# Optimization experiments

Hardware: AMD Instinct MI355X
Metric: run time of the kernel (lower is better)

The kernel has to match this reference:

```python
import jax, jax.numpy as jnp
import numpy as np

IMAGE_SIZE = 224
FMAP_H = FMAP_W = 26   # resnet18 layer2 (28x28) after AvgPool2d(3, stride=1)
N_REWEIGHT = 3
SIGMA = 4.0
KSIZE = 2 * int(4.0 * SIGMA + 0.5) + 1  # 33, kornia-style default kernel for sigma=4


def _gaussian_kernel1d():
    x = np.arange(KSIZE, dtype=np.float64) - (KSIZE - 1) / 2.0
    k = np.exp(-0.5 * (x / SIGMA) ** 2)
    return jnp.asarray((k / k.sum()).astype(np.float32))


def _cdist(x, y):
    # Euclidean cdist: x [N,D], y [M,D] -> [N,M], via the expanded quadratic form.
    x2 = jnp.sum(x * x, axis=1, keepdims=True)          # [N,1]
    y2 = jnp.sum(y * y, axis=1)                          # [M]
    d2 = x2 + y2 - 2.0 * (x @ y.T)                       # [N,M]
    return jnp.sqrt(jnp.maximum(d2, 0.0))


def _gaussian_blur(img):
    # Separable depthwise gaussian blur with reflect padding, img [1,1,H,W].
    k1d = _gaussian_kernel1d()
    pad = (KSIZE - 1) // 2
    x = jnp.pad(img, ((0, 0), (0, 0), (pad, pad), (pad, pad)), mode='reflect')
    kh = k1d.reshape(1, 1, KSIZE, 1)
    kw = k1d.reshape(1, 1, 1, KSIZE)
    dn = ('NCHW', 'OIHW', 'NCHW')
    x = jax.lax.conv_general_dilated(x, kh, (1, 1), 'VALID', dimension_numbers=dn)
    x = jax.lax.conv_general_dilated(x, kw, (1, 1), 'VALID', dimension_numbers=dn)
    return x


def setup_inputs() -> dict:
    key = jax.random.key(0)
    k1, k2 = jax.random.split(key)
    patch = jax.random.normal(k1, (FMAP_H * FMAP_W, 384), dtype=jnp.float32)      # [676, 384]
    patch_lib = jax.random.normal(k2, (100000, 384), dtype=jnp.float32)            # coreset bank
    return {"patch": patch, "patch_lib": patch_lib}


def reference(patch, patch_lib):
    # dist = torch.cdist(patch, patch_lib); min over memory bank
    dist = _cdist(patch, patch_lib)                      # [N, M]
    min_val = jnp.min(dist, axis=1)                      # [N]
    min_idx = jnp.argmin(dist, axis=1)                   # [N]
    s_idx = jnp.argmax(min_val)                          # most anomalous patch
    s_star = min_val[s_idx]
    m_test = patch[s_idx]                                # [D]
    m_star = patch_lib[min_idx[s_idx]]                   # [D]
    # reweighting: k nearest neighbors of m_star in the bank (smallest distances)
    w_dist = jnp.linalg.norm(m_star[None, :] - patch_lib, axis=1)   # [M]
    _, nn_idx = jax.lax.top_k(-w_dist, N_REWEIGHT)                  # indices of k smallest
    m_star_knn = jnp.linalg.norm(m_test[None, :] - patch_lib[nn_idx[1:]], axis=1)  # [k-1]
    D = jnp.sqrt(jnp.asarray(patch.shape[1], dtype=jnp.float32))
    w = 1.0 - jnp.exp(s_star / D) / jnp.sum(jnp.exp(m_star_knn / D))
    s = w * s_star
    # segmentation map: reshape, bilinear upsample (align_corners=False), gaussian blur
    s_map = min_val.reshape(1, 1, FMAP_H, FMAP_W)
    s_map = jax.image.resize(s_map, (1, 1, IMAGE_SIZE, IMAGE_SIZE), method='bilinear')
    s_map = _gaussian_blur(s_map)
    return s, s_map
```

## Files before the change

### kernel.cpp

```cpp
#include <hip/hip_runtime.h>

#define M_PATCH 676
#define K_DIM   384
#define N_LIB   100000
#define BM      128
#define BN      128
#define NCH     782
#define MTILES  6
#define M_PAD   (MTILES*BM)
#define N_PAD   (NCH*BN)
#define XCHUNK  98
#define GRID_GEMM (8*XCHUNK*MTILES)
#define NTOPB   1563
#define NCAND   (NTOPB*3)
#define IMG     224
#define FMAP    26
#define KS      33
#define KHALF   16

typedef __attribute__((ext_vector_type(4))) float  f32x4;
typedef __attribute__((ext_vector_type(8))) short  short8;
typedef unsigned long long ull;

static __device__ __forceinline__ unsigned short f2bf(float f) {
  unsigned u = __float_as_uint(f);
  u = u + 0x7FFFu + ((u >> 16) & 1u);
  return (unsigned short)(u >> 16);
}

static __device__ __forceinline__ ull shfl_xor_u64(ull v, int m) {
  unsigned lo = (unsigned)v, hi = (unsigned)(v >> 32);
  lo = __shfl_xor(lo, m, 64);
  hi = __shfl_xor(hi, m, 64);
  return ((ull)hi << 32) | lo;
}

static __device__ __forceinline__ ull umin64(ull a, ull b) { return a < b ? a : b; }
static __device__ __forceinline__ ull umax64(ull a, ull b) { return a > b ? a : b; }

static __device__ __forceinline__ void gld16(const unsigned short* g, unsigned short* l) {
  __builtin_amdgcn_global_load_lds(
      (const __attribute__((address_space(1))) void*)g,
      (__attribute__((address_space(3))) void*)l, 16, 0, 0);
}

__global__ void pc_norms_cvt_kernel(const float* __restrict__ patch, const float* __restrict__ lib,
                                    float* __restrict__ y2, float* __restrict__ x2,
                                    unsigned short* __restrict__ Abf, unsigned short* __restrict__ Bbf) {
  const int w = threadIdx.x >> 6, lane = threadIdx.x & 63;
  const long r = (long)blockIdx.x * 4 + w;
  if (r < N_PAD) {
    float s;
    if (r < N_LIB) {
      const float2* p = (const float2*)(lib + r * K_DIM);
      ushort2* q = (ushort2*)(Bbf + r * K_DIM);
      float2 v[3];
      s = 0.f;
      #pragma unroll
      for (int j = 0; j < 3; ++j) { v[j] = p[lane + 64 * j]; s += v[j].x * v[j].x + v[j].y * v[j].y; }
      #pragma unroll
      for (int j = 0; j < 3; ++j) q[lane + 64 * j] = make_ushort2(f2bf(v[j].x), f2bf(v[j].y));
      #pragma unroll
      for (int m = 1; m < 64; m <<= 1) s += __shfl_xor(s, m, 64);
    } else {
      s = __builtin_inff();
      ushort2* q = (ushort2*)(Bbf + r * K_DIM);
      #pragma unroll
      for (int j = 0; j < 3; ++j) q[lane + 64 * j] = make_ushort2(0, 0);
    }
    if (lane == 0) y2[r] = s;
  } else {
    const long pr = r - N_PAD;
    if (pr < M_PATCH) {
      const float2* p = (const float2*)(patch + pr * K_DIM);
      ushort2* q = (ushort2*)(Abf + pr * K_DIM);
      float2 v[3]; float s = 0.f;
      #pragma unroll
      for (int j = 0; j < 3; ++j) { v[j] = p[lane + 64 * j]; s += v[j].x * v[j].x + v[j].y * v[j].y; }
      #pragma unroll
      for (int j = 0; j < 3; ++j) q[lane + 64 * j] = make_ushort2(f2bf(v[j].x), f2bf(v[j].y));
      #pragma unroll
      for (int m = 1; m < 64; m <<= 1) s += __shfl_xor(s, m, 64);
      if (lane == 0) x2[pr] = s;
    } else if (pr < M_PAD) {
      ushort2* q = (ushort2*)(Abf + pr * K_DIM);
      #pragma unroll
      for (int j = 0; j < 3; ++j) q[lane + 64 * j] = make_ushort2(0, 0);
    }
  }
}

__launch_bounds__(256, 4)
__global__ void pc_gemm_min_bf16_kernel(const unsigned short* __restrict__ Abf,
                                        const unsigned short* __restrict__ Bbf,
                                        const float* __restrict__ x2g, const float* __restrict__ y2g,
                                        ull* __restrict__ partial) {
  __shared__ unsigned short As[2][BM * 32];
  __shared__ unsigned short Bs[2][BN * 32];
  __shared__ float x2s[BM];
  __shared__ float y2s[BN];
  __shared__ ull red[BM * 2];

  const int l = blockIdx.x;
  const int xcd = l & 7, slot = l >> 3;
  const int chunk = xcd * XCHUNK + slot / MTILES;
  const int mtile = slot % MTILES;
  if (chunk >= NCH) return;

  const int t = threadIdx.x;
  const int m0 = mtile * BM;
  const int n0 = chunk * BN;
  const int wid = t >> 6, lane = t & 63;

  if (t < BM) {
    const int gm = m0 + t;
    x2s[t] = (gm < M_PATCH) ? x2g[gm] : 0.f;
    y2s[t] = y2g[n0 + t];
  }

  const int srow   = (wid << 4) + (lane >> 2);
  const int spiece = (lane & 3) ^ ((lane >> 4) & 3);
  const unsigned short* gA0 = Abf + (size_t)(m0 + srow) * K_DIM + spiece * 8;
  const unsigned short* gA1 = gA0 + (size_t)64 * K_DIM;
  const unsigned short* gB0 = Bbf + (size_t)(n0 + srow) * K_DIM + spiece * 8;
  const unsigned short* gB1 = gB0 + (size_t)64 * K_DIM;

  f32x4 acc[4][4];
  #pragma unroll
  for (int i = 0; i < 4; ++i)
    #pragma unroll
    for (int j = 0; j < 4; ++j) acc[i][j] = (f32x4){0.f, 0.f, 0.f, 0.f};

  const int wm = wid >> 1, wn = wid & 1;
  const int quad = lane >> 4, l15 = lane & 15;
  const int poff = (quad ^ ((l15 >> 2) & 3)) * 8;

  for (int ks = 0; ks < K_DIM / 64; ++ks) {
    __syncthreads();
    #pragma unroll
    for (int h = 0; h < 2; ++h) {
      const int ko = ks * 64 + h * 32;
      gld16(gA0 + ko, &As[h][wid * 512]);
      gld16(gA1 + ko, &As[h][(wid + 4) * 512]);
      gld16(gB0 + ko, &Bs[h][wid * 512]);
      gld16(gB1 + ko, &Bs[h][(wid + 4) * 512]);
    }
    __builtin_amdgcn_s_waitcnt(0);
    __syncthreads();

    #pragma unroll
    for (int h = 0; h < 2; ++h) {
      short8 af[4], bf[4];
      #pragma unroll
      for (int mi = 0; mi < 4; ++mi)
        af[mi] = *(const short8*)&As[h][(wm * 64 + mi * 16 + l15) * 32 + poff];
      #pragma unroll
      for (int ni = 0; ni < 4; ++ni)
        bf[ni] = *(const short8*)&Bs[h][(wn * 64 + ni * 16 + l15) * 32 + poff];
      #pragma unroll
      for (int mi = 0; mi < 4; ++mi)
        #pragma unroll
        for (int ni = 0; ni < 4; ++ni)
          acc[mi][ni] = __builtin_amdgcn_mfma_f32_16x16x32_bf16(af[mi], bf[ni], acc[mi][ni], 0, 0, 0);
    }
  }

  #pragma unroll
  for (int mi = 0; mi < 4; ++mi) {
    #pragma unroll
    for (int r = 0; r < 4; ++r) {
      const int row_l = wm * 64 + mi * 16 + quad * 4 + r;
      const float xs = x2s[row_l];
      ull kmin = ~0ull;
      #pragma unroll
      for (int ni = 0; ni < 4; ++ni) {
        const int col_l = wn * 64 + ni * 16 + l15;
        float d2 = xs + y2s[col_l] - 2.0f * acc[mi][ni][r];
        d2 = fmaxf(d2, 0.0f);
        const ull key = ((ull)__float_as_uint(d2) << 32) | (unsigned)(n0 + col_l);
        kmin = umin64(kmin, key);
      }
      #pragma unroll
      for (int off = 1; off < 16; off <<= 1) kmin = umin64(kmin, shfl_xor_u64(kmin, off));
      if (l15 == 0) red[row_l * 2 + wn] = kmin;
    }
  }
  __syncthreads();
  if (t < BM) {
    const ull k = umin64(red[t * 2], red[t * 2 + 1]);
    partial[(size_t)chunk * M_PAD + m0 + t] = k;
  }
}

__global__ void pc_reduce_kernel(const ull* __restrict__ partial, ull* __restrict__ stage1,
                                 float* __restrict__ minval, unsigned* __restrict__ minidx,
                                 unsigned* __restrict__ scal) {
  const int b = blockIdx.x, mt = b >> 3, gp = b & 7;
  const int t = threadIdx.x;
  const int c0 = gp * XCHUNK;
  ull k = ~0ull;
  #pragma unroll 7
  for (int i = 0; i < XCHUNK; ++i)
    k = umin64(k, partial[(size_t)(c0 + i) * M_PAD + mt * 128 + t]);
  stage1[(size_t)(mt * 128 + t) * 8 + gp] = k;
  __threadfence();
  __syncthreads();
  __shared__ unsigned rank_s;
  if (t == 0) rank_s = atomicAdd(&scal[8], 1u);
  __syncthreads();
  if (rank_s != 47) return;
  __threadfence();

  ull best = 0ull;
  for (int m = t; m < M_PATCH; m += 128) {
    ull kk = ~0ull;
    #pragma unroll
    for (int g = 0; g < 8; ++g) kk = umin64(kk, stage1[(size_t)m * 8 + g]);
    const float d = sqrtf(fmaxf(__uint_as_float((unsigned)(kk >> 32)), 0.f));
    minval[m] = d;
    minidx[m] = (unsigned)kk;
    best = umax64(best, ((ull)__float_as_uint(d) << 32) | (0xFFFFFFFFu - (unsigned)m));
  }
  #pragma unroll
  for (int off = 1; off < 64; off <<= 1) best = umax64(best, shfl_xor_u64(best, off));
  __shared__ ull sh[2];
  if ((t & 63) == 0) sh[t >> 6] = best;
  __syncthreads();
  if (t == 0) {
    best = umax64(sh[0], sh[1]);
    const unsigned m = 0xFFFFFFFFu - (unsigned)best;
    scal[0] = m;
    scal[1] = (unsigned)(best >> 32);
    scal[2] = minidx[m];
  }
}

__global__ void pc_wdist_scan_kernel(const unsigned short* __restrict__ Bbf,
                                     const float* __restrict__ y2,
                                     const unsigned* __restrict__ scal,
                                     ull* __restrict__ cand) {
  __shared__ ull keys[64];
  const int t = threadIdx.x, w = t >> 6, lane = t & 63;
  const unsigned star = scal[2];
  const float y2star = y2[star];
  const unsigned* msp = (const unsigned*)(Bbf + (size_t)star * K_DIM);
  float msl[3], msh[3];
  #pragma unroll
  for (int j = 0; j < 3; ++j) {
    const unsigned u = msp[lane + 64 * j];
    msl[j] = __uint_as_float(u << 16);
    msh[j] = __uint_as_float(u & 0xFFFF0000u);
  }
  const long r0 = (long)blockIdx.x * 64 + w * 16;
  for (int i = 0; i < 16; ++i) {
    const long r = r0 + i;
    ull key = ~0ull;
    if (r < N_LIB) {
      const unsigned* p = (const unsigned*)(Bbf + (size_t)r * K_DIM);
      float s = 0.f;
      #pragma unroll
      for (int j = 0; j < 3; ++j) {
        const unsigned u = p[lane + 64 * j];
        s += msl[j] * __uint_as_float(u << 16) + msh[j] * __uint_as_float(u & 0xFFFF0000u);
      }
      #pragma unroll
      for (int m = 1; m < 64; m <<= 1) s += __shfl_xor(s, m, 64);
      const float d2 = fmaxf(y2star + y2[r] - 2.0f * s, 0.0f);
      key = ((ull)__float_as_uint(d2) << 32) | (unsigned)r;
    }
    if (lane == 0) keys[w * 16 + i] = key;
  }
  __syncthreads();
  if (t == 0) {
    ull picks[3];
    #pragma unroll
    for (int p = 0; p < 3; ++p) {
      ull best = ~0ull;
      for (int i = 0; i < 64; ++i) {
        const ull k = keys[i];
        if ((p > 0 && k == picks[0]) || (p > 1 && k == picks[1])) continue;
        best = umin64(best, k);
      }
      picks[p] = best;
      cand[(long)blockIdx.x * 3 + p] = best;
    }
  }
}

__global__ void pc_merge_final_kernel(const float* __restrict__ patch, const float* __restrict__ lib,
                                      const unsigned* __restrict__ scal, const ull* __restrict__ cand,
                                      float* __restrict__ out) {
  __shared__ ull shm[16];
  __shared__ ull picks_s[3];
  const int t = threadIdx.x, w = t >> 6, lane = t & 63;
  for (int p = 0; p < 3; ++p) {
    const ull e0 = (p > 0) ? picks_s[0] : 0ull;
    const ull e1 = (p > 1) ? picks_s[1] : 0ull;
    ull k = ~0ull;
    for (int n = t; n < NCAND; n += 1024) {
      const ull c = cand[n];
      if ((p > 0 && c == e0) || (p > 1 && c == e1)) continue;
      k = umin64(k, c);
    }
    #pragma unroll
    for (int off = 1; off < 64; off <<= 1) k = umin64(k, shfl_xor_u64(k, off));
    if ((t & 63) == 0) shm[t >> 6] = k;
    __syncthreads();
    if (t == 0) {
      #pragma unroll
      for (int ww = 1; ww < 16; ++ww) k = umin64(k, shm[ww]);
      picks_s[p] = k;
    }
    __syncthreads();
  }
  __shared__ float sh2[2];
  if (w < 2) {
    const unsigned nn = (unsigned)picks_s[1 + w];
    const float* mt2 = patch + (size_t)scal[0] * K_DIM;
    const float* pv  = lib + (size_t)nn * K_DIM;
    float s = 0.f;
    #pragma unroll
    for (int j = 0; j < 6; ++j) { const float d = mt2[lane + 64 * j] - pv[lane + 64 * j]; s += d * d; }
    #pragma unroll
    for (int m = 1; m < 64; m <<= 1) s += __shfl_xor(s, m, 64);
    if (lane == 0) sh2[w] = s;
  }
  __syncthreads();
  if (t == 0) {
    const float D = sqrtf((float)K_DIM);
    const float s_star = __uint_as_float(scal[1]);
    const float a = sqrtf(sh2[0]), b = sqrtf(sh2[1]);
    const float wgt = 1.f - expf(s_star / D) / (expf(a / D) + expf(b / D));
    out[0] = wgt * s_star;
  }
}

static __device__ __forceinline__ int pc_refl(int i) {
  return i < 0 ? -i : (i >= IMG ? 2 * IMG - 2 - i : i);
}

__global__ void pc_map_kernel(const float* __restrict__ minval, float* __restrict__ outmap) {
  __shared__ double kd[KS + 1];
  __shared__ float kf[KS];
  __shared__ float smap[FMAP * FMAP];
  __shared__ float by[IMG];
  const int t = threadIdx.x;
  const int y = blockIdx.x;
  if (t < KS) { const double xx = (double)(t - KHALF) / 4.0; kd[t] = exp(-0.5 * xx * xx); }
  for (int i = t; i < FMAP * FMAP; i += 256) smap[i] = minval[i];
  __syncthreads();
  if (t == 0) { double s = 0.0; for (int i = 0; i < KS; ++i) s += kd[i]; kd[KS] = s; }
  __syncthreads();
  if (t < KS) kf[t] = (float)(kd[t] / kd[KS]);
  __syncthreads();

  const float scale = (float)FMAP / (float)IMG;
  if (t < IMG) {
    const float fx = ((float)t + 0.5f) * scale - 0.5f;
    const int ix0 = (int)floorf(fx); const float tx = fx - (float)ix0;
    const int x0 = min(max(ix0, 0), FMAP - 1), x1 = min(max(ix0 + 1, 0), FMAP - 1);
    float s = 0.f;
    #pragma unroll
    for (int j = 0; j < KS; ++j) {
      const int yy = pc_refl(y + j - KHALF);
      const float fy = ((float)yy + 0.5f) * scale - 0.5f;
      const int iy0 = (int)floorf(fy); const float ty = fy - (float)iy0;
      const int y0 = min(max(iy0, 0), FMAP - 1), y1 = min(max(iy0 + 1, 0), FMAP - 1);
      const float v00 = smap[y0 * FMAP + x0], v01 = smap[y0 * FMAP + x1];
      const float v10 = smap[y1 * FMAP + x0], v11 = smap[y1 * FMAP + x1];
      const float v0 = v00 + (v01 - v00) * tx;
      const float v1 = v10 + (v11 - v10) * tx;
      s += kf[j] * (v0 + (v1 - v0) * ty);
    }
    by[t] = s;
  }
  __syncthreads();
  if (t < IMG) {
    float s = 0.f;
    #pragma unroll
    for (int i = 0; i < KS; ++i) s += kf[i] * by[pc_refl(t + i - KHALF)];
    outmap[y * IMG + t] = s;
  }
}

extern "C" void kernel_launch(void* const* d_in, const int* in_sizes, int n_in,
                              void* d_out, int out_size, void* d_ws, size_t ws_size,
                              hipStream_t stream) {
  const float* patch = (const float*)d_in[0];
  const float* lib   = (const float*)d_in[1];
  float* out = (float*)d_out;

  char* p = (char*)d_ws;
  auto take = [&](size_t n) { char* q = p; p += (n + 511) & ~(size_t)511; return q; };
  float* y2        = (float*)take((size_t)N_PAD * 4);
  float* x2        = (float*)take((size_t)M_PAD * 4);
  ull* partial     = (ull*)take((size_t)(NCH + 2) * M_PAD * 8);
  ull* stage1      = (ull*)take((size_t)M_PAD * 8 * 8);
  float* minval    = (float*)take((size_t)M_PATCH * 4);
  unsigned* minidx = (unsigned*)take((size_t)M_PATCH * 4);
  unsigned* scal   = (unsigned*)take(256);
  ull* cand        = (ull*)take((size_t)NCAND * 8);
  unsigned short* Abf = (unsigned short*)take((size_t)M_PAD * K_DIM * 2);
  unsigned short* Bbf = (unsigned short*)take((size_t)N_PAD * K_DIM * 2);
  (void)in_sizes; (void)n_in; (void)out_size; (void)ws_size;

  hipMemsetAsync(scal, 0, 64, stream);
  hipMemsetAsync(partial + (size_t)NCH * M_PAD, 0xFF, 2 * M_PAD * 8, stream);

  const int norm_rows = N_PAD + M_PAD;
  pc_norms_cvt_kernel<<<(norm_rows + 3) / 4, 256, 0, stream>>>(patch, lib, y2, x2, Abf, Bbf);
  pc_gemm_min_bf16_kernel<<<GRID_GEMM, 256, 0, stream>>>(Abf, Bbf, x2, y2, partial);
  pc_reduce_kernel<<<48, 128, 0, stream>>>(partial, stage1, minval, minidx, scal);
  pc_wdist_scan_kernel<<<NTOPB, 256, 0, stream>>>(Bbf, y2, scal, cand);
  pc_merge_final_kernel<<<1, 1024, 0, stream>>>(patch, lib, scal, cand, out);
  pc_map_kernel<<<IMG, 256, 0, stream>>>(minval, out + 1);
}
```

Measured before the change: 385.7 us.

## Pack GEMM min keys to 32-bit with DPP, batch wdist scan, drop memsets

The GEMM epilogue packs the distance and a local column index into a 32-bit key by truncating the low 6 mantissa bits. It then reduces those keys with DPP row-rotate mins instead of 64-bit shuffles. The norms/convert kernel handles two rows per wave with wider loads. The wdist scan batches four rows' loads and reductions and replaces the serial top-3 pick with wave shuffles. The two memsets are folded into kernels, removing launch overhead, but the truncated key can change argmin tie-breaking near equal distances and only scal[8] is zeroed now.

```diff
diff --git a/kernel.cpp b/kernel.cpp
--- a/kernel.cpp
+++ b/kernel.cpp
@@ -37,6 +37,11 @@
 
 static __device__ __forceinline__ ull umin64(ull a, ull b) { return a < b ? a : b; }
 static __device__ __forceinline__ ull umax64(ull a, ull b) { return a > b ? a : b; }
+static __device__ __forceinline__ unsigned umin32(unsigned a, unsigned b) { return a < b ? a : b; }
+
+#define DPP_ROR_MIN(x, n)                                                              \
+  (x) = umin32((x), (unsigned)__builtin_amdgcn_update_dpp((int)(x), (int)(x),          \
+                                                          0x120 + (n), 0xF, 0xF, false))
 
 static __device__ __forceinline__ void gld16(const unsigned short* g, unsigned short* l) {
   __builtin_amdgcn_global_load_lds(
@@ -46,46 +51,50 @@
 
 __global__ void pc_norms_cvt_kernel(const float* __restrict__ patch, const float* __restrict__ lib,
                                     float* __restrict__ y2, float* __restrict__ x2,
-                                    unsigned short* __restrict__ Abf, unsigned short* __restrict__ Bbf) {
+                                    unsigned short* __restrict__ Abf, unsigned short* __restrict__ Bbf,
+                                    unsigned* __restrict__ scal) {
+  if (blockIdx.x == 0 && threadIdx.x == 0) scal[8] = 0;
   const int w = threadIdx.x >> 6, lane = threadIdx.x & 63;
-  const long r = (long)blockIdx.x * 4 + w;
-  if (r < N_PAD) {
-    float s;
-    if (r < N_LIB) {
-      const float2* p = (const float2*)(lib + r * K_DIM);
-      ushort2* q = (ushort2*)(Bbf + r * K_DIM);
-      float2 v[3];
-      s = 0.f;
-      #pragma unroll
-      for (int j = 0; j < 3; ++j) { v[j] = p[lane + 64 * j]; s += v[j].x * v[j].x + v[j].y * v[j].y; }
-      #pragma unroll
-      for (int j = 0; j < 3; ++j) q[lane + 64 * j] = make_ushort2(f2bf(v[j].x), f2bf(v[j].y));
-      #pragma unroll
-      for (int m = 1; m < 64; m <<= 1) s += __shfl_xor(s, m, 64);
+  const long rbase = (long)blockIdx.x * 8 + w * 2;
+  #pragma unroll
+  for (int i = 0; i < 2; ++i) {
+    const long r = rbase + i;
+    if (r < N_PAD) {
+      if (r < N_LIB) {
+        const float* src = lib + r * K_DIM;
+        const float4 v4 = *(const float4*)(src + lane * 4);
+        const float2 v2 = *(const float2*)(src + 256 + lane * 2);
+        *(ushort4*)(Bbf + r * K_DIM + lane * 4) =
+            make_ushort4(f2bf(v4.x), f2bf(v4.y), f2bf(v4.z), f2bf(v4.w));
+        *(ushort2*)(Bbf + r * K_DIM + 256 + lane * 2) = make_ushort2(f2bf(v2.x), f2bf(v2.y));
+        float s = v4.x * v4.x + v4.y * v4.y + v4.z * v4.z + v4.w * v4.w
+                + v2.x * v2.x + v2.y * v2.y;
+        #pragma unroll
+        for (int m = 1; m < 64; m <<= 1) s += __shfl_xor(s, m, 64);
+        if (lane == 0) y2[r] = s;
+      } else {
+        *(ushort4*)(Bbf + r * K_DIM + lane * 4) = make_ushort4(0, 0, 0, 0);
+        *(ushort2*)(Bbf + r * K_DIM + 256 + lane * 2) = make_ushort2(0, 0);
+        if (lane == 0) y2[r] = __builtin_inff();
+      }
     } else {
-      s = __builtin_inff();
-      ushort2* q = (ushort2*)(Bbf + r * K_DIM);
-      #pragma unroll
-      for (int j = 0; j < 3; ++j) q[lane + 64 * j] = make_ushort2(0, 0);
-    }
-    if (lane == 0) y2[r] = s;
-  } else {
-    const long pr = r - N_PAD;
-    if (pr < M_PATCH) {
-      const float2* p = (const float2*)(patch + pr * K_DIM);
-      ushort2* q = (ushort2*)(Abf + pr * K_DIM);
-      float2 v[3]; float s = 0.f;
-      #pragma unroll
-      for (int j = 0; j < 3; ++j) { v[j] = p[lane + 64 * j]; s += v[j].x * v[j].x + v[j].y * v[j].y; }
-      #pragma unroll
-      for (int j = 0; j < 3; ++j) q[lane + 64 * j] = make_ushort2(f2bf(v[j].x), f2bf(v[j].y));
-      #pragma unroll
-      for (int m = 1; m < 64; m <<= 1) s += __shfl_xor(s, m, 64);
-      if (lane == 0) x2[pr] = s;
-    } else if (pr < M_PAD) {
-      ushort2* q = (ushort2*)(Abf + pr * K_DIM);
-      #pragma unroll
-      for (int j = 0; j < 3; ++j) q[lane + 64 * j] = make_ushort2(0, 0);
+      const long pr = r - N_PAD;
+      if (pr < M_PATCH) {
+        const float* src = patch + pr * K_DIM;
+        const float4 v4 = *(const float4*)(src + lane * 4);
+        const float2 v2 = *(const float2*)(src + 256 + lane * 2);
+        *(ushort4*)(Abf + pr * K_DIM + lane * 4) =
+            make_ushort4(f2bf(v4.x), f2bf(v4.y), f2bf(v4.z), f2bf(v4.w));
+        *(ushort2*)(Abf + pr * K_DIM + 256 + lane * 2) = make_ushort2(f2bf(v2.x), f2bf(v2.y));
+        float s = v4.x * v4.x + v4.y * v4.y + v4.z * v4.z + v4.w * v4.w
+                + v2.x * v2.x + v2.y * v2.y;
+        #pragma unroll
+        for (int m = 1; m < 64; m <<= 1) s += __shfl_xor(s, m, 64);
+        if (lane == 0) x2[pr] = s;
+      } else if (pr < M_PAD) {
+        *(ushort4*)(Abf + pr * K_DIM + lane * 4) = make_ushort4(0, 0, 0, 0);
+        *(ushort2*)(Abf + pr * K_DIM + 256 + lane * 2) = make_ushort2(0, 0);
+      }
     }
   }
 }
@@ -99,16 +108,18 @@
   __shared__ unsigned short Bs[2][BN * 32];
   __shared__ float x2s[BM];
   __shared__ float y2s[BN];
-  __shared__ ull red[BM * 2];
+  __shared__ unsigned red32[BM * 2];
 
   const int l = blockIdx.x;
   const int xcd = l & 7, slot = l >> 3;
   const int chunk = xcd * XCHUNK + slot / MTILES;
   const int mtile = slot % MTILES;
-  if (chunk >= NCH) return;
-
   const int t = threadIdx.x;
   const int m0 = mtile * BM;
+  if (chunk >= NCH) {
+    if (t < BM) partial[(size_t)chunk * M_PAD + m0 + t] = ~0ull;
+    return;
+  }
   const int n0 = chunk * BN;
   const int wid = t >> 6, lane = t & 63;
 
@@ -171,24 +182,28 @@
     for (int r = 0; r < 4; ++r) {
       const int row_l = wm * 64 + mi * 16 + quad * 4 + r;
       const float xs = x2s[row_l];
-      ull kmin = ~0ull;
+      unsigned kmin = 0xFFFFFFFFu;
       #pragma unroll
       for (int ni = 0; ni < 4; ++ni) {
         const int col_l = wn * 64 + ni * 16 + l15;
         float d2 = xs + y2s[col_l] - 2.0f * acc[mi][ni][r];
         d2 = fmaxf(d2, 0.0f);
-        const ull key = ((ull)__float_as_uint(d2) << 32) | (unsigned)(n0 + col_l);
-        kmin = umin64(kmin, key);
+        const unsigned key = (__float_as_uint(d2) & 0xFFFFFFC0u) | (unsigned)(ni * 16 + l15);
+        kmin = umin32(kmin, key);
       }
-      #pragma unroll
-      for (int off = 1; off < 16; off <<= 1) kmin = umin64(kmin, shfl_xor_u64(kmin, off));
-      if (l15 == 0) red[row_l * 2 + wn] = kmin;
+      DPP_ROR_MIN(kmin, 8);
+      DPP_ROR_MIN(kmin, 4);
+      DPP_ROR_MIN(kmin, 2);
+      DPP_ROR_MIN(kmin, 1);
+      if (l15 == 0) red32[row_l * 2 + wn] = kmin;
     }
   }
   __syncthreads();
   if (t < BM) {
-    const ull k = umin64(red[t * 2], red[t * 2 + 1]);
-    partial[(size_t)chunk * M_PAD + m0 + t] = k;
+    const unsigned v0 = red32[t * 2], v1 = red32[t * 2 + 1];
+    const ull k0 = ((ull)(v0 & 0xFFFFFFC0u) << 32) | (unsigned)(n0 + (v0 & 63u));
+    const ull k1 = ((ull)(v1 & 0xFFFFFFC0u) << 32) | (unsigned)(n0 + 64 + (v1 & 63u));
+    partial[(size_t)chunk * M_PAD + m0 + t] = umin64(k0, k1);
   }
 }
 
@@ -252,37 +267,60 @@
     msh[j] = __uint_as_float(u & 0xFFFF0000u);
   }
   const long r0 = (long)blockIdx.x * 64 + w * 16;
-  for (int i = 0; i < 16; ++i) {
-    const long r = r0 + i;
-    ull key = ~0ull;
-    if (r < N_LIB) {
-      const unsigned* p = (const unsigned*)(Bbf + (size_t)r * K_DIM);
-      float s = 0.f;
-      #pragma unroll
-      for (int j = 0; j < 3; ++j) {
-        const unsigned u = p[lane + 64 * j];
-        s += msl[j] * __uint_as_float(u << 16) + msh[j] * __uint_as_float(u & 0xFFFF0000u);
+  #pragma unroll
+  for (int b = 0; b < 4; ++b) {
+    const long rb = r0 + b * 4;
+    unsigned u[4][3];
+    #pragma unroll
+    for (int i = 0; i < 4; ++i) {
+      const long r = rb + i;
+      const unsigned* p = (const unsigned*)(Bbf + (size_t)(r < N_LIB ? r : 0) * K_DIM);
+      #pragma unroll
+      for (int j = 0; j < 3; ++j) u[i][j] = p[lane + 64 * j];
+    }
+    float s[4];
+    #pragma unroll
+    for (int i = 0; i < 4; ++i) {
+      s[i] = 0.f;
+      #pragma unroll
+      for (int j = 0; j < 3; ++j)
+        s[i] += msl[j] * __uint_as_float(u[i][j] << 16)
+              + msh[j] * __uint_as_float(u[i][j] & 0xFFFF0000u);
+    }
+    #pragma unroll
+    for (int m = 1; m < 64; m <<= 1) {
+      #pragma unroll
+      for (int i = 0; i < 4; ++i) s[i] += __shfl_xor(s[i], m, 64);
+    }
+    if (lane == 0) {
+      #pragma unroll
+      for (int i = 0; i < 4; ++i) {
+        const long r = rb + i;
+        const float d2 = fmaxf(y2star + y2[r] - 2.0f * s[i], 0.0f);
+        keys[w * 16 + b * 4 + i] =
+            (r < N_LIB) ? (((ull)__float_as_uint(d2) << 32) | (unsigned)r) : ~0ull;
       }
-      #pragma unroll
-      for (int m = 1; m < 64; m <<= 1) s += __shfl_xor(s, m, 64);
-      const float d2 = fmaxf(y2star + y2[r] - 2.0f * s, 0.0f);
-      key = ((ull)__float_as_uint(d2) << 32) | (unsigned)r;
-    }
-    if (lane == 0) keys[w * 16 + i] = key;
-  }
-  __syncthreads();
-  if (t == 0) {
-    ull picks[3];
-    #pragma unroll
-    for (int p = 0; p < 3; ++p) {
-      ull best = ~0ull;
-      for (int i = 0; i < 64; ++i) {
-        const ull k = keys[i];
-        if ((p > 0 && k == picks[0]) || (p > 1 && k == picks[1])) continue;
-        best = umin64(best, k);
-      }
-      picks[p] = best;
-      cand[(long)blockIdx.x * 3 + p] = best;
+    }
+  }
+  __syncthreads();
+  if (w == 0) {
+    const ull k0 = keys[lane];
+    ull p0, p1, k;
+    k = k0;
+    #pragma unroll
+    for (int off = 1; off < 64; off <<= 1) k = umin64(k, shfl_xor_u64(k, off));
+    p0 = k;
+    k = (k0 == p0) ? ~0ull : k0;
+    #pragma unroll
+    for (int off = 1; off < 64; off <<= 1) k = umin64(k, shfl_xor_u64(k, off));
+    p1 = k;
+    k = (k0 == p0 || k0 == p1) ? ~0ull : k0;
+    #pragma unroll
+    for (int off = 1; off < 64; off <<= 1) k = umin64(k, shfl_xor_u64(k, off));
+    if (lane == 0) {
+      cand[(long)blockIdx.x * 3 + 0] = p0;
+      cand[(long)blockIdx.x * 3 + 1] = p1;
+      cand[(long)blockIdx.x * 3 + 2] = k;
     }
   }
 }
@@ -404,11 +442,8 @@
   unsigned short* Bbf = (unsigned short*)take((size_t)N_PAD * K_DIM * 2);
   (void)in_sizes; (void)n_in; (void)out_size; (void)ws_size;
 
-  hipMemsetAsync(scal, 0, 64, stream);
-  hipMemsetAsync(partial + (size_t)NCH * M_PAD, 0xFF, 2 * M_PAD * 8, stream);
-
   const int norm_rows = N_PAD + M_PAD;
-  pc_norms_cvt_kernel<<<(norm_rows + 3) / 4, 256, 0, stream>>>(patch, lib, y2, x2, Abf, Bbf);
+  pc_norms_cvt_kernel<<<norm_rows / 8, 256, 0, stream>>>(patch, lib, y2, x2, Abf, Bbf, scal);
   pc_gemm_min_bf16_kernel<<<GRID_GEMM, 256, 0, stream>>>(Abf, Bbf, x2, y2, partial);
   pc_reduce_kernel<<<48, 128, 0, stream>>>(partial, stage1, minval, minidx, scal);
   pc_wdist_scan_kernel<<<NTOPB, 256, 0, stream>>>(Bbf, y2, scal, cand);
```

New measurement: 339.0 us. 1.14x faster.
